# Kernel optimization log

Hardware: AMD Instinct MI355X
Metric: run time of the kernel (lower is better)

Reference implementation:

```python
import jax, jax.numpy as jnp
import numpy as np

BETA_MIN = 0.01
BETA_MAX = 0.995
EPS = 1e-6


def setup_inputs() -> dict:
    key = jax.random.key(0)
    k1, k2, k3, k4 = jax.random.split(key, 4)
    B, T, D = 16, 4096, 128
    return {
        "q": jax.random.normal(k1, (B, T, D), dtype=jnp.float32),
        "k": jax.random.normal(k2, (B, T, D), dtype=jnp.float32),
        "v": jax.random.normal(k3, (B, T, D), dtype=jnp.float32),
        "beta": jax.random.uniform(k4, (B, T, 1), dtype=jnp.float32),
        "mask": jnp.ones((B, T, 1), dtype=jnp.float32),
        "base_beta_1": jnp.asarray(2.0, dtype=jnp.float32),
        "base_beta_2": jnp.asarray(3.0, dtype=jnp.float32),
    }


def _delta_scan(q, k, v, beta, mask, base_beta_1, base_beta_2):
    B, T, D = q.shape
    phi_q = jax.nn.elu(q) + 1.0  # positive feature map
    phi_k = jax.nn.elu(k) + 1.0
    b1_base = jnp.clip(jax.nn.sigmoid(base_beta_1), BETA_MIN, BETA_MAX)
    b2_base = jnp.clip(jax.nn.sigmoid(base_beta_2), BETA_MIN, BETA_MAX)

    # time-major for scan: [T, B, ...]
    xs = (
        jnp.swapaxes(phi_q, 0, 1),
        jnp.swapaxes(phi_k, 0, 1),
        jnp.swapaxes(v, 0, 1),
        jnp.swapaxes(beta, 0, 1),
        jnp.swapaxes(mask, 0, 1),
    )

    H1 = jnp.zeros((B, D, D), dtype=q.dtype)
    H2 = jnp.zeros((B, D, D), dtype=q.dtype)
    Z1 = jnp.zeros((B, D), dtype=q.dtype)
    Z2 = jnp.zeros((B, D), dtype=q.dtype)

    def step(carry, x):
        H1, H2, Z1, Z2 = carry
        q_t, k_t, v_t, b_in_t, m_t = x  # q_t:[B,D], b_in_t/m_t:[B,1]
        b_in_t = jnp.clip(b_in_t, BETA_MIN, BETA_MAX)
        b1_t = jnp.clip(b1_base * b_in_t, BETA_MIN, BETA_MAX)  # [B,1]
        b2_t = jnp.clip(b2_base * b_in_t, BETA_MIN, BETA_MAX)
        kv = jnp.einsum('bd,be->bde', k_t, v_t) * m_t[:, :, None]  # masked outer product
        H1 = H1 * b1_t[:, :, None] + kv
        H2 = H2 * b2_t[:, :, None] + kv
        Z1 = Z1 * b1_t + k_t * m_t
        Z2 = Z2 * b2_t + k_t * m_t
        num = jnp.einsum('bd,bde->be', q_t, H1 + H2)
        den = jnp.maximum(jnp.sum(q_t * (Z1 + Z2), axis=-1, keepdims=True), EPS)
        o_t = num / den * m_t
        return (H1, H2, Z1, Z2), o_t

    _, outs = jax.lax.scan(step, (H1, H2, Z1, Z2), xs)
    return jnp.swapaxes(outs, 0, 1)  # [B, T, D]


def reference(q, k, v, beta, mask, base_beta_1, base_beta_2):
    return _delta_scan(q, k, v, beta, mask, base_beta_1, base_beta_2)
```

## Files before the change

### kernel.cpp

```cpp
#include <hip/hip_runtime.h>

#define B_ 16
#define T_ 4096
#define D_ 128
#define L_ 128
#define NC_ 32
#define CH_ (B_*NC_)
#define LDP 136

typedef __attribute__((ext_vector_type(8))) short bf16x8;
typedef __attribute__((ext_vector_type(4))) float f32x4;

__device__ __forceinline__ float clampf(float x, float lo, float hi) {
    return fminf(fmaxf(x, lo), hi);
}
__device__ __forceinline__ float phi_f(float x) {
    return x > 0.f ? x + 1.f : __expf(x);
}
__device__ __forceinline__ unsigned short bf16r(float f) {
    unsigned u = __builtin_bit_cast(unsigned, f);
    u += 0x7FFFu + ((u >> 16) & 1u);
    return (unsigned short)(u >> 16);
}
__device__ __forceinline__ float fbf(unsigned short h) {
    unsigned u = ((unsigned)h) << 16; return __builtin_bit_cast(float, u);
}
__device__ __forceinline__ unsigned pack2bf(float a, float b) {
    return (unsigned)bf16r(a) | ((unsigned)bf16r(b) << 16);
}
__device__ __forceinline__ uint4 pack8(const float* f) {
    uint4 r;
    r.x = pack2bf(f[0], f[1]); r.y = pack2bf(f[2], f[3]);
    r.z = pack2bf(f[4], f[5]); r.w = pack2bf(f[6], f[7]);
    return r;
}
__device__ __forceinline__ f32x4 zero4() { f32x4 z; z[0]=0.f; z[1]=0.f; z[2]=0.f; z[3]=0.f; return z; }

__device__ __forceinline__ int aidx(int row, int k0) {
    return (((row >> 4) * 4 + (k0 >> 5)) * 64 + ((k0 >> 3) & 3) * 16 + (row & 15)) * 8;
}

__global__ void k0w(const float* __restrict__ beta,
                    const float* __restrict__ bb1, const float* __restrict__ bb2,
                    float* __restrict__ lg1, float* __restrict__ lg2,
                    float* __restrict__ wexp) {
    int ch = blockIdx.x;
    int b = ch / NC_, c = ch % NC_;
    int tbase = b * T_ + c * L_;
    int tid = threadIdx.x;
    int lane = tid & 63, w = tid >> 6;
    __shared__ float tot1s[2], tot2s[2];

    float b1b = clampf(1.f / (1.f + __expf(-bb1[0])), 0.01f, 0.995f);
    float b2b = clampf(1.f / (1.f + __expf(-bb2[0])), 0.01f, 0.995f);
    float be = clampf(beta[tbase + tid], 0.01f, 0.995f);
    float x1 = __logf(clampf(b1b * be, 0.01f, 0.995f));
    float x2 = __logf(clampf(b2b * be, 0.01f, 0.995f));
#pragma unroll
    for (int off = 1; off < 64; off <<= 1) {
        float y1 = __shfl_up(x1, off);
        float y2 = __shfl_up(x2, off);
        if (lane >= off) { x1 += y1; x2 += y2; }
    }
    if (lane == 63) { tot1s[w] = x1; tot2s[w] = x2; }
    __syncthreads();
    if (w == 1) { x1 += tot1s[0]; x2 += tot2s[0]; }
    float tot1 = tot1s[0] + tot1s[1];
    float tot2 = tot2s[0] + tot2s[1];
    lg1[tbase + tid] = x1;
    lg2[tbase + tid] = x2;
    wexp[(size_t)ch * 128 + tid]                     = __expf(tot1 - x1);
    wexp[(size_t)CH_ * 128 + (size_t)ch * 128 + tid] = __expf(tot2 - x2);
}

__global__ __launch_bounds__(256) void kS(
        const float* __restrict__ kk, const float* __restrict__ vv,
        const float* __restrict__ mask,
        unsigned short* __restrict__ phiKT, unsigned short* __restrict__ VtT) {
    int g = blockIdx.x;
    int ch = g >> 2, q = g & 3;
    int b = ch / NC_, c = ch % NC_;
    int tbase = b * T_ + c * L_;
    int tid = threadIdx.x;
    size_t cb = (size_t)ch * 16384;

#pragma unroll
    for (int p = 0; p < 2; ++p) {
        int i = p * 256 + tid;
        int s = q * 32 + (i >> 4), d0 = (i & 15) * 8;
        const float* kp = &kk[(size_t)(tbase + s) * D_ + d0];
        float4 x0 = *(const float4*)kp, x1 = *(const float4*)(kp + 4);
        float m = mask[tbase + s];
        float pq[8] = {phi_f(x0.x)*m, phi_f(x0.y)*m, phi_f(x0.z)*m, phi_f(x0.w)*m,
                       phi_f(x1.x)*m, phi_f(x1.y)*m, phi_f(x1.z)*m, phi_f(x1.w)*m};
        *(uint4*)&phiKT[cb + aidx(s, d0)] = pack8(pq);
    }

#pragma unroll
    for (int p = 0; p < 2; ++p) {
        int i = p * 256 + tid;
        int e = q * 32 + (i & 31), s0 = (i >> 5) * 8;
        const float* vp = &vv[(size_t)(tbase + s0) * D_ + e];
        float f[8];
#pragma unroll
        for (int j = 0; j < 8; ++j)
            f[j] = vp[(size_t)j * D_];
        *(uint4*)&VtT[cb + aidx(e, s0)] = pack8(f);
    }
}

__global__ __launch_bounds__(256, 2) void kC(
        const float* __restrict__ kk, const float* __restrict__ mask,
        const unsigned short* __restrict__ VtT, const float* __restrict__ wexp,
        unsigned short* __restrict__ Cws, float* __restrict__ zc) {
    int ch = blockIdx.x;
    int b = ch / NC_, c = ch % NC_;
    int tbase = b * T_ + c * L_;
    int tid = threadIdx.x, lane = tid & 63, w = tid >> 6;
    int l15 = lane & 15, lg4 = lane >> 4;
    size_t cb = (size_t)ch * 16384;
    __shared__ unsigned short sKt[16384];

#pragma unroll
    for (int p = 0; p < 8; ++p) {
        int i = p * 256 + tid;
        int d = i & 127, s0 = (i >> 7) * 8;
        const float* kp = &kk[(size_t)(tbase + s0) * D_ + d];
        const float* mp = &mask[tbase + s0];
        float f[8];
#pragma unroll
        for (int j = 0; j < 8; ++j)
            f[j] = phi_f(kp[(size_t)j * D_]) * mp[j];
        *(uint4*)&sKt[aidx(d, s0)] = pack8(f);
    }
    __syncthreads();

    const float* wp0 = &wexp[(size_t)ch * 128];
    const float* wp1 = &wexp[(size_t)CH_ * 128 + (size_t)ch * 128];

    f32x4 acc[2][2][8];
#pragma unroll
    for (int st = 0; st < 2; ++st)
#pragma unroll
        for (int mm = 0; mm < 2; ++mm)
#pragma unroll
            for (int n = 0; n < 8; ++n) acc[st][mm][n] = zero4();
    float zp[2][8];
#pragma unroll
    for (int st = 0; st < 2; ++st)
#pragma unroll
        for (int n = 0; n < 8; ++n) zp[st][n] = 0.f;

#pragma unroll
    for (int ks = 0; ks < 4; ++ks) {
        int koff = ks * 32 + lg4 * 8;
        float wl0[8], wl1[8];
        {
            float4 a0 = *(const float4*)&wp0[koff];
            float4 a1 = *(const float4*)&wp0[koff + 4];
            float4 b0 = *(const float4*)&wp1[koff];
            float4 b1 = *(const float4*)&wp1[koff + 4];
            wl0[0]=a0.x; wl0[1]=a0.y; wl0[2]=a0.z; wl0[3]=a0.w;
            wl0[4]=a1.x; wl0[5]=a1.y; wl0[6]=a1.z; wl0[7]=a1.w;
            wl1[0]=b0.x; wl1[1]=b0.y; wl1[2]=b0.z; wl1[3]=b0.w;
            wl1[4]=b1.x; wl1[5]=b1.y; wl1[6]=b1.z; wl1[7]=b1.w;
        }
        bf16x8 as0[2], as1[2];
#pragma unroll
        for (int mm = 0; mm < 2; ++mm) {
            bf16x8 vt = *(const bf16x8*)&VtT[cb + (size_t)((((w * 2 + mm) * 4 + ks) * 64 + lane) * 8)];
#pragma unroll
            for (int j = 0; j < 8; ++j) {
                float av = fbf((unsigned short)vt[j]);
                as0[mm][j] = (short)bf16r(av * wl0[j]);
                as1[mm][j] = (short)bf16r(av * wl1[j]);
            }
        }
        bf16x8 bb[8];
#pragma unroll
        for (int n = 0; n < 8; ++n)
            bb[n] = *(const bf16x8*)&sKt[((n * 4 + ks) * 64 + lane) * 8];
        if (w == 0) {
#pragma unroll
            for (int n = 0; n < 8; ++n)
#pragma unroll
                for (int j = 0; j < 8; ++j) {
                    float kv = fbf((unsigned short)bb[n][j]);
                    zp[0][n] += wl0[j] * kv;
                    zp[1][n] += wl1[j] * kv;
                }
        }
#pragma unroll
        for (int n = 0; n < 8; ++n) {
            acc[0][0][n] = __builtin_amdgcn_mfma_f32_16x16x32_bf16(as0[0], bb[n], acc[0][0][n], 0, 0, 0);
            acc[0][1][n] = __builtin_amdgcn_mfma_f32_16x16x32_bf16(as0[1], bb[n], acc[0][1][n], 0, 0, 0);
            acc[1][0][n] = __builtin_amdgcn_mfma_f32_16x16x32_bf16(as1[0], bb[n], acc[1][0][n], 0, 0, 0);
            acc[1][1][n] = __builtin_amdgcn_mfma_f32_16x16x32_bf16(as1[1], bb[n], acc[1][1][n], 0, 0, 0);
        }
    }

    if (w == 0) {
#pragma unroll
        for (int st = 0; st < 2; ++st)
#pragma unroll
            for (int n = 0; n < 8; ++n) {
                float z = zp[st][n];
                z += __shfl_xor(z, 16); z += __shfl_xor(z, 32);
                if (lg4 == 0)
                    zc[((size_t)(st * B_ + b) * NC_ + c) * D_ + n * 16 + l15] = z;
            }
    }

    __syncthreads();
#pragma unroll
    for (int st = 0; st < 2; ++st) {
#pragma unroll
        for (int mm = 0; mm < 2; ++mm)
#pragma unroll
            for (int n = 0; n < 8; ++n)
#pragma unroll
                for (int r = 0; r < 4; ++r) {
                    int e = (w * 2 + mm) * 16 + lg4 * 4 + r;
                    int d = n * 16 + l15;
                    sKt[aidx(e, d & ~7) + (d & 7)] = bf16r(acc[st][mm][n][r]);
                }
        __syncthreads();
        unsigned short* Cp = Cws + ((size_t)(st * B_ + b) * NC_ + c) * (D_ * D_);
#pragma unroll
        for (int p = 0; p < 8; ++p) {
            int i = tid + p * 256;
            *(uint4*)&Cp[(size_t)i * 8] = *(const uint4*)&sKt[i * 8];
        }
        if (st == 0) __syncthreads();
    }
}

__global__ void k2f(unsigned short* __restrict__ Cws, float* __restrict__ zc,
                    const float* __restrict__ lg1, const float* __restrict__ lg2) {
    int g = blockIdx.x * blockDim.x + threadIdx.x;
    if (g < 131072) {
        int st = g >> 16;
        int rem = g & 65535;
        int b = rem >> 12;
        int de = (rem & 4095) * 4;
        const float* lg = st ? lg2 : lg1;
        size_t base = ((size_t)(st * B_ + b) * NC_) * (D_ * D_) + de;
        float run0 = 0.f, run1 = 0.f, run2 = 0.f, run3 = 0.f;
        for (int c = 0; c < NC_; c++) {
            float a = __expf(lg[b * T_ + c * L_ + L_ - 1]);
            uint2 val = *(uint2*)&Cws[base + (size_t)c * (D_ * D_)];
            float t0 = fbf((unsigned short)(val.x & 0xffff)), t1 = fbf((unsigned short)(val.x >> 16));
            float t2 = fbf((unsigned short)(val.y & 0xffff)), t3 = fbf((unsigned short)(val.y >> 16));
            uint2 wv; wv.x = pack2bf(run0, run1); wv.y = pack2bf(run2, run3);
            *(uint2*)&Cws[base + (size_t)c * (D_ * D_)] = wv;
            run0 = a * run0 + t0; run1 = a * run1 + t1;
            run2 = a * run2 + t2; run3 = a * run3 + t3;
        }
    } else {
        int gz = g - 131072;
        int st = gz >> 11;
        int rem = gz & 2047;
        int b = rem >> 7;
        int d = rem & 127;
        const float* lg = st ? lg2 : lg1;
        size_t base = ((size_t)(st * B_ + b) * NC_) * D_ + d;
        float run = 0.f;
        for (int c = 0; c < NC_; c++) {
            float a = __expf(lg[b * T_ + c * L_ + L_ - 1]);
            float tmp = zc[base + (size_t)c * D_];
            zc[base + (size_t)c * D_] = run;
            run = a * run + tmp;
        }
    }
}

__global__ __launch_bounds__(512, 4) void k3_v7(
        const float* __restrict__ qq, const float* __restrict__ mask,
        const float* __restrict__ lg1, const float* __restrict__ lg2,
        const unsigned short* __restrict__ phiKT, const unsigned short* __restrict__ VtT,
        const unsigned short* __restrict__ Cws, const float* __restrict__ zc,
        float* __restrict__ out) {
    __shared__ unsigned short bufP[8][16 * LDP];
    int ch = blockIdx.x;
    int b = ch / NC_, c = ch % NC_;
    int tbase = b * T_ + c * L_;
    int tid = threadIdx.x, lane = tid & 63, w = tid >> 6;
    int l15 = lane & 15, lg4 = lane >> 4;
    unsigned short* bufPw = &bufP[w][0];
    size_t cb = (size_t)ch * 16384;

    int trow = w * 16 + l15;
    size_t gt = (size_t)(tbase + trow);

    float lg1t = lg1[gt], lg2t = lg2[gt], mt = mask[gt];
    float a1t = __expf(lg1t), a2t = __expf(lg2t);

    bf16x8 qf[4];
#pragma unroll
    for (int ks = 0; ks < 4; ++ks) {
        int koff = ks * 32 + lg4 * 8;
        const float* qp = &qq[gt * D_ + koff];
        float4 x0 = *(const float4*)qp, x1 = *(const float4*)(qp + 4);
        float p0[8] = {phi_f(x0.x), phi_f(x0.y), phi_f(x0.z), phi_f(x0.w),
                       phi_f(x1.x), phi_f(x1.y), phi_f(x1.z), phi_f(x1.w)};
#pragma unroll
        for (int j = 0; j < 8; ++j) qf[ks][j] = (short)bf16r(p0[j]);
    }

    const float* z1p = &zc[((size_t)(0 * B_ + b) * NC_ + c) * D_];
    const float* z2p = &zc[((size_t)(1 * B_ + b) * NC_ + c) * D_];
    float d1 = 0.f, d2 = 0.f;
#pragma unroll
    for (int ks = 0; ks < 4; ++ks) {
        int off = ks * 32 + lg4 * 8;
        float4 za = *(const float4*)(z1p + off), zb = *(const float4*)(z1p + off + 4);
        float4 zca = *(const float4*)(z2p + off), zcb = *(const float4*)(z2p + off + 4);
        float z1a[8] = {za.x, za.y, za.z, za.w, zb.x, zb.y, zb.z, zb.w};
        float z2a[8] = {zca.x, zca.y, zca.z, zca.w, zcb.x, zcb.y, zcb.z, zcb.w};
#pragma unroll
        for (int j = 0; j < 8; ++j) {
            float fq = fbf((unsigned short)qf[ks][j]);
            d1 += fq * z1a[j]; d2 += fq * z2a[j];
        }
    }
    d1 += __shfl_xor(d1, 16); d1 += __shfl_xor(d1, 32);
    d2 += __shfl_xor(d2, 16); d2 += __shfl_xor(d2, 32);

    int SN = (w | 1) + 1;
    int KP = SN >> 1;
    float rs = 0.f;
    for (int sp = 0; sp < KP; ++sp) {
        bf16x8 kf[8];
#pragma unroll
        for (int mm = 0; mm < 2; ++mm)
#pragma unroll
            for (int ks = 0; ks < 4; ++ks)
                kf[mm * 4 + ks] = *(const bf16x8*)&phiKT[cb + (size_t)(((((sp * 2 + mm) * 4) + ks) * 64 + lane) * 8)];
        f32x4 accs[2];
        accs[0] = zero4(); accs[1] = zero4();
#pragma unroll
        for (int ks = 0; ks < 4; ++ks)
#pragma unroll
            for (int mm = 0; mm < 2; ++mm)
                accs[mm] = __builtin_amdgcn_mfma_f32_16x16x32_bf16(kf[mm * 4 + ks], qf[ks], accs[mm], 0, 0, 0);
#pragma unroll
        for (int mm = 0; mm < 2; ++mm) {
            int s0 = (sp * 2 + mm) * 16 + lg4 * 4;
            float4 l1s = *(const float4*)&lg1[tbase + s0];
            float4 l2s = *(const float4*)&lg2[tbase + s0];
            float l1a[4] = {l1s.x, l1s.y, l1s.z, l1s.w};
            float l2a[4] = {l2s.x, l2s.y, l2s.z, l2s.w};
            float pv[4];
#pragma unroll
            for (int r = 0; r < 4; ++r) {
                int s = s0 + r;
                float p = 0.f;
                if (s <= trow)
                    p = accs[mm][r] * (__expf(lg1t - l1a[r]) + __expf(lg2t - l2a[r]));
                pv[r] = p; rs += p;
            }
            uint2 dd; dd.x = pack2bf(pv[0], pv[1]); dd.y = pack2bf(pv[2], pv[3]);
            *(uint2*)&bufPw[l15 * LDP + s0] = dd;
        }
    }
    rs += __shfl_xor(rs, 16); rs += __shfl_xor(rs, 32);
    float osc = mt / fmaxf(a1t * d1 + a2t * d2 + rs, 1e-6f);

    f32x4 acc_o[8];
#pragma unroll
    for (int m = 0; m < 8; ++m) acc_o[m] = zero4();
#pragma unroll
    for (int st = 0; st < 2; ++st) {
        const unsigned short* Hp = Cws + ((size_t)(st * B_ + b) * NC_ + c) * (D_ * D_);
        float sc = st ? a2t : a1t;
#pragma unroll
        for (int ks = 0; ks < 4; ++ks) {
            bf16x8 hf[8];
#pragma unroll
            for (int m = 0; m < 8; ++m)
                hf[m] = *(const bf16x8*)&Hp[(size_t)(((m * 4 + ks) * 64 + lane) * 8)];
            bf16x8 qs;
#pragma unroll
            for (int j = 0; j < 8; ++j)
                qs[j] = (short)bf16r(fbf((unsigned short)qf[ks][j]) * sc);
#pragma unroll
            for (int m = 0; m < 8; ++m)
                acc_o[m] = __builtin_amdgcn_mfma_f32_16x16x32_bf16(hf[m], qs, acc_o[m], 0, 0, 0);
        }
    }

    for (int ks = 0; ks < KP; ++ks) {
        bf16x8 vf[8];
#pragma unroll
        for (int m = 0; m < 8; ++m)
            vf[m] = *(const bf16x8*)&VtT[cb + (size_t)(((m * 4 + ks) * 64 + lane) * 8)];
        bf16x8 pf = *(const bf16x8*)&bufPw[l15 * LDP + ks * 32 + lg4 * 8];
#pragma unroll
        for (int m = 0; m < 8; ++m)
            acc_o[m] = __builtin_amdgcn_mfma_f32_16x16x32_bf16(vf[m], pf, acc_o[m], 0, 0, 0);
    }

#pragma unroll
    for (int m = 0; m < 8; ++m) {
        float4 o;
        o.x = acc_o[m][0] * osc; o.y = acc_o[m][1] * osc;
        o.z = acc_o[m][2] * osc; o.w = acc_o[m][3] * osc;
        *(float4*)&out[gt * D_ + m * 16 + lg4 * 4] = o;
    }
}

extern "C" void kernel_launch(void* const* d_in, const int* in_sizes, int n_in,
                              void* d_out, int out_size, void* d_ws, size_t ws_size,
                              hipStream_t stream) {
    const float* q    = (const float*)d_in[0];
    const float* k    = (const float*)d_in[1];
    const float* v    = (const float*)d_in[2];
    const float* beta = (const float*)d_in[3];
    const float* mask = (const float*)d_in[4];
    const float* bb1  = (const float*)d_in[5];
    const float* bb2  = (const float*)d_in[6];
    float* out = (float*)d_out;

    size_t n_lg = (size_t)B_ * T_;
    size_t n_z  = (size_t)2 * B_ * NC_ * D_;
    size_t n_w  = (size_t)2 * CH_ * 128;
    size_t n_C  = (size_t)2 * B_ * NC_ * D_ * D_;
    size_t n_kt = (size_t)B_ * T_ * D_;
    size_t need = (2 * n_lg + n_z + n_w) * sizeof(float) + (n_C + 2 * n_kt) * sizeof(unsigned short);
    if (ws_size < need) return;

    float* lg1  = (float*)d_ws;
    float* lg2  = lg1 + n_lg;
    float* zc   = lg2 + n_lg;
    float* wexp = zc + n_z;
    unsigned short* Cws    = (unsigned short*)(wexp + n_w);
    unsigned short* phiKT  = Cws + n_C;
    unsigned short* VtT    = phiKT + n_kt;

    k0w<<<CH_, 128, 0, stream>>>(beta, bb1, bb2, lg1, lg2, wexp);
    kS<<<4 * CH_, 256, 0, stream>>>(k, v, mask, phiKT, VtT);
    kC<<<CH_, 256, 0, stream>>>(k, mask, VtT, wexp, Cws, zc);
    k2f<<<528, 256, 0, stream>>>(Cws, zc, lg1, lg2);
    k3_v7<<<CH_, 512, 0, stream>>>(q, mask, lg1, lg2, phiKT, VtT, Cws, zc, out);
}
```

Baseline: 89.98 us.

## Split chunk-state kernel across the two decay streams with 512-thread blocks

```diff
diff --git a/kernel.cpp b/kernel.cpp
--- a/kernel.cpp
+++ b/kernel.cpp
@@ -109,11 +109,13 @@
     }
 }
 
-__global__ __launch_bounds__(256, 2) void kC(
+__global__ __launch_bounds__(512, 4) void kC(
         const float* __restrict__ kk, const float* __restrict__ mask,
         const unsigned short* __restrict__ VtT, const float* __restrict__ wexp,
         unsigned short* __restrict__ Cws, float* __restrict__ zc) {
-    int ch = blockIdx.x;
+    int g = blockIdx.x;
+    int ch = ((g >> 4) << 3) | (g & 7);
+    int st = (g >> 3) & 1;
     int b = ch / NC_, c = ch % NC_;
     int tbase = b * T_ + c * L_;
     int tid = threadIdx.x, lane = tid & 63, w = tid >> 6;
@@ -122,8 +124,8 @@
     __shared__ unsigned short sKt[16384];
 
 #pragma unroll
-    for (int p = 0; p < 8; ++p) {
-        int i = p * 256 + tid;
+    for (int p = 0; p < 4; ++p) {
+        int i = p * 512 + tid;
         int d = i & 127, s0 = (i >> 7) * 8;
         const float* kp = &kk[(size_t)(tbase + s0) * D_ + d];
         const float* mp = &mask[tbase + s0];
@@ -135,46 +137,29 @@
     }
     __syncthreads();
 
-    const float* wp0 = &wexp[(size_t)ch * 128];
-    const float* wp1 = &wexp[(size_t)CH_ * 128 + (size_t)ch * 128];
-
-    f32x4 acc[2][2][8];
-#pragma unroll
-    for (int st = 0; st < 2; ++st)
-#pragma unroll
-        for (int mm = 0; mm < 2; ++mm)
-#pragma unroll
-            for (int n = 0; n < 8; ++n) acc[st][mm][n] = zero4();
-    float zp[2][8];
-#pragma unroll
-    for (int st = 0; st < 2; ++st)
-#pragma unroll
-        for (int n = 0; n < 8; ++n) zp[st][n] = 0.f;
+    const float* wp = &wexp[(size_t)st * CH_ * 128 + (size_t)ch * 128];
+
+    f32x4 acc[8];
+#pragma unroll
+    for (int n = 0; n < 8; ++n) acc[n] = zero4();
+    float zp[8] = {0.f, 0.f, 0.f, 0.f, 0.f, 0.f, 0.f, 0.f};
 
 #pragma unroll
     for (int ks = 0; ks < 4; ++ks) {
         int koff = ks * 32 + lg4 * 8;
-        float wl0[8], wl1[8];
+        float wl[8];
         {
-            float4 a0 = *(const float4*)&wp0[koff];
-            float4 a1 = *(const float4*)&wp0[koff + 4];
-            float4 b0 = *(const float4*)&wp1[koff];
-            float4 b1 = *(const float4*)&wp1[koff + 4];
-            wl0[0]=a0.x; wl0[1]=a0.y; wl0[2]=a0.z; wl0[3]=a0.w;
-            wl0[4]=a1.x; wl0[5]=a1.y; wl0[6]=a1.z; wl0[7]=a1.w;
-            wl1[0]=b0.x; wl1[1]=b0.y; wl1[2]=b0.z; wl1[3]=b0.w;
-            wl1[4]=b1.x; wl1[5]=b1.y; wl1[6]=b1.z; wl1[7]=b1.w;
-        }
-        bf16x8 as0[2], as1[2];
-#pragma unroll
-        for (int mm = 0; mm < 2; ++mm) {
-            bf16x8 vt = *(const bf16x8*)&VtT[cb + (size_t)((((w * 2 + mm) * 4 + ks) * 64 + lane) * 8)];
-#pragma unroll
-            for (int j = 0; j < 8; ++j) {
-                float av = fbf((unsigned short)vt[j]);
-                as0[mm][j] = (short)bf16r(av * wl0[j]);
-                as1[mm][j] = (short)bf16r(av * wl1[j]);
-            }
+            float4 a0 = *(const float4*)&wp[koff];
+            float4 a1 = *(const float4*)&wp[koff + 4];
+            wl[0]=a0.x; wl[1]=a0.y; wl[2]=a0.z; wl[3]=a0.w;
+            wl[4]=a1.x; wl[5]=a1.y; wl[6]=a1.z; wl[7]=a1.w;
+        }
+        bf16x8 as;
+        {
+            bf16x8 vt = *(const bf16x8*)&VtT[cb + (size_t)(((w * 4 + ks) * 64 + lane) * 8)];
+#pragma unroll
+            for (int j = 0; j < 8; ++j)
+                as[j] = (short)bf16r(fbf((unsigned short)vt[j]) * wl[j]);
         }
         bf16x8 bb[8];
 #pragma unroll
@@ -184,54 +169,39 @@
 #pragma unroll
             for (int n = 0; n < 8; ++n)
 #pragma unroll
-                for (int j = 0; j < 8; ++j) {
-                    float kv = fbf((unsigned short)bb[n][j]);
-                    zp[0][n] += wl0[j] * kv;
-                    zp[1][n] += wl1[j] * kv;
-                }
-        }
+                for (int j = 0; j < 8; ++j)
+                    zp[n] += wl[j] * fbf((unsigned short)bb[n][j]);
+        }
+#pragma unroll
+        for (int n = 0; n < 8; ++n)
+            acc[n] = __builtin_amdgcn_mfma_f32_16x16x32_bf16(as, bb[n], acc[n], 0, 0, 0);
+    }
+
+    if (w == 0) {
 #pragma unroll
         for (int n = 0; n < 8; ++n) {
-            acc[0][0][n] = __builtin_amdgcn_mfma_f32_16x16x32_bf16(as0[0], bb[n], acc[0][0][n], 0, 0, 0);
-            acc[0][1][n] = __builtin_amdgcn_mfma_f32_16x16x32_bf16(as0[1], bb[n], acc[0][1][n], 0, 0, 0);
-            acc[1][0][n] = __builtin_amdgcn_mfma_f32_16x16x32_bf16(as1[0], bb[n], acc[1][0][n], 0, 0, 0);
-            acc[1][1][n] = __builtin_amdgcn_mfma_f32_16x16x32_bf16(as1[1], bb[n], acc[1][1][n], 0, 0, 0);
-        }
-    }
-
-    if (w == 0) {
-#pragma unroll
-        for (int st = 0; st < 2; ++st)
-#pragma unroll
-            for (int n = 0; n < 8; ++n) {
-                float z = zp[st][n];
-                z += __shfl_xor(z, 16); z += __shfl_xor(z, 32);
-                if (lg4 == 0)
-                    zc[((size_t)(st * B_ + b) * NC_ + c) * D_ + n * 16 + l15] = z;
-            }
+            float z = zp[n];
+            z += __shfl_xor(z, 16); z += __shfl_xor(z, 32);
+            if (lg4 == 0)
+                zc[((size_t)(st * B_ + b) * NC_ + c) * D_ + n * 16 + l15] = z;
+        }
     }
 
     __syncthreads();
 #pragma unroll
-    for (int st = 0; st < 2; ++st) {
-#pragma unroll
-        for (int mm = 0; mm < 2; ++mm)
-#pragma unroll
-            for (int n = 0; n < 8; ++n)
-#pragma unroll
-                for (int r = 0; r < 4; ++r) {
-                    int e = (w * 2 + mm) * 16 + lg4 * 4 + r;
-                    int d = n * 16 + l15;
-                    sKt[aidx(e, d & ~7) + (d & 7)] = bf16r(acc[st][mm][n][r]);
-                }
-        __syncthreads();
-        unsigned short* Cp = Cws + ((size_t)(st * B_ + b) * NC_ + c) * (D_ * D_);
-#pragma unroll
-        for (int p = 0; p < 8; ++p) {
-            int i = tid + p * 256;
-            *(uint4*)&Cp[(size_t)i * 8] = *(const uint4*)&sKt[i * 8];
-        }
-        if (st == 0) __syncthreads();
+    for (int n = 0; n < 8; ++n)
+#pragma unroll
+        for (int r = 0; r < 4; ++r) {
+            int e = w * 16 + lg4 * 4 + r;
+            int d = n * 16 + l15;
+            sKt[aidx(e, d & ~7) + (d & 7)] = bf16r(acc[n][r]);
+        }
+    __syncthreads();
+    unsigned short* Cp = Cws + ((size_t)(st * B_ + b) * NC_ + c) * (D_ * D_);
+#pragma unroll
+    for (int p = 0; p < 4; ++p) {
+        int i = p * 512 + tid;
+        *(uint4*)&Cp[(size_t)i * 8] = *(const uint4*)&sKt[i * 8];
     }
 }
 
@@ -246,6 +216,7 @@
         const float* lg = st ? lg2 : lg1;
         size_t base = ((size_t)(st * B_ + b) * NC_) * (D_ * D_) + de;
         float run0 = 0.f, run1 = 0.f, run2 = 0.f, run3 = 0.f;
+#pragma unroll
         for (int c = 0; c < NC_; c++) {
             float a = __expf(lg[b * T_ + c * L_ + L_ - 1]);
             uint2 val = *(uint2*)&Cws[base + (size_t)c * (D_ * D_)];
@@ -265,6 +236,7 @@
         const float* lg = st ? lg2 : lg1;
         size_t base = ((size_t)(st * B_ + b) * NC_) * D_ + d;
         float run = 0.f;
+#pragma unroll
         for (int c = 0; c < NC_; c++) {
             float a = __expf(lg[b * T_ + c * L_ + L_ - 1]);
             float tmp = zc[base + (size_t)c * D_];
@@ -439,7 +411,7 @@
 
     k0w<<<CH_, 128, 0, stream>>>(beta, bb1, bb2, lg1, lg2, wexp);
     kS<<<4 * CH_, 256, 0, stream>>>(k, v, mask, phiKT, VtT);
-    kC<<<CH_, 256, 0, stream>>>(k, mask, VtT, wexp, Cws, zc);
+    kC<<<2 * CH_, 512, 0, stream>>>(k, mask, VtT, wexp, Cws, zc);
     k2f<<<528, 256, 0, stream>>>(Cws, zc, lg1, lg2);
     k3_v7<<<CH_, 512, 0, stream>>>(q, mask, lg1, lg2, phiKT, VtT, Cws, zc, out);
 }
```

Result: no change. 91.77 us (+2.0%).
